# Optimization experiments

Measured on AMD Instinct MI355X. Metric: run time of the kernel, lower is better.

Reference implementation:

```python
import jax, jax.numpy as jnp
import numpy as np

NUM_HEADS = 64  # init kwarg


def _split_heads(x, num_heads):
    # torch: x.view(N, num_heads, head_size).permute(0, 2, 1) -> [N, head_size, num_heads]
    n, hidden = x.shape
    head_size = hidden // num_heads
    return x.reshape(n, num_heads, head_size).transpose(0, 2, 1)


def setup_inputs() -> dict:
    key = jax.random.key(0)
    kq, kk, kv = jax.random.split(key, 3)
    N, H = 4096, 4096
    q = jax.random.normal(kq, (N, H), dtype=jnp.float32)
    k = jax.random.normal(kk, (N, H), dtype=jnp.float32)
    v = jax.random.normal(kv, (N, H), dtype=jnp.float32)
    return {"q": q, "k": k, "v": v}


def reference(q, k, v):
    n, hidden = q.shape
    qh = _split_heads(q, NUM_HEADS)  # [N, d, h] with d=head_size, h=num_heads
    kh = _split_heads(k, NUM_HEADS)
    vh = _split_heads(v, NUM_HEADS)
    # scores: contraction over the num_heads axis (faithful to the original code)
    scores = jnp.einsum('ndh,neh->nde', qh, kh)      # [N, d, d]
    probs = jax.nn.softmax(scores, axis=-1)           # softmax over last dim, no scaling
    out = jnp.einsum('nde,neh->ndh', probs, vh)       # [N, d, h]
    # permute(0,2,1) then flatten -> [N, hidden]
    return out.transpose(0, 2, 1).reshape(n, hidden)
```

## Files before the change

kernel.cpp:

```cpp
#include <hip/hip_runtime.h>
#include <hip/hip_bf16.h>

typedef __bf16 bf16x8 __attribute__((ext_vector_type(8)));
typedef float  f32x4  __attribute__((ext_vector_type(4)));
typedef short  s16x8  __attribute__((ext_vector_type(8)));
typedef unsigned short u16;

static __device__ __forceinline__ u16 f2bf_rne(float f) {
  union { float f; unsigned u; } x; x.f = f;
  unsigned r = x.u + 0x7fffu + ((x.u >> 16) & 1u);
  return (u16)(r >> 16);
}

static __device__ __forceinline__ void splitbf(float f, short& hi, short& lo) {
  union { float f; unsigned u; } x; x.f = f;
  hi = (short)(x.u >> 16);
  union { unsigned u; float f; } h; h.u = x.u & 0xffff0000u;
  union { float f; unsigned u; } y; y.f = f - h.f;
  lo = (short)(y.u >> 16);
}

__global__ __launch_bounds__(256, 2)
void attn64_kernel(const float* __restrict__ q, const float* __restrict__ k,
                   const float* __restrict__ v, float* __restrict__ out)
{
  __shared__ u16 plds[4][4608];
  const int tid  = threadIdx.x;
  const int wid  = tid >> 6;
  const int lane = tid & 63;
  const int quad = lane >> 4;
  const int lo   = lane & 15;
  const int row  = blockIdx.x * 4 + wid;

  u16* P = plds[wid];
  const float* qrow = q + (size_t)row * 4096;
  const float* krow = k + (size_t)row * 4096;
  const float* vrow = v + (size_t)row * 4096;
  float*       orow = out + (size_t)row * 4096;

  const int hq = quad * 8;

  float xk[8][8];
#pragma unroll
  for (int ks = 0; ks < 2; ++ks)
#pragma unroll
    for (int et = 0; et < 4; ++et)
#pragma unroll
      for (int j = 0; j < 8; ++j)
        xk[ks * 4 + et][j] = krow[(ks * 32 + hq + j) * 64 + lo + 16 * et];

  s16x8 kh[8], kl[8];
#pragma unroll
  for (int i = 0; i < 8; ++i)
#pragma unroll
    for (int j = 0; j < 8; ++j) {
      short h0, l0; splitbf(xk[i][j], h0, l0);
      kh[i][j] = h0; kl[i][j] = l0;
    }

  float xq[8][8];
#pragma unroll
  for (int ks = 0; ks < 2; ++ks)
#pragma unroll
    for (int dt = 0; dt < 4; ++dt)
#pragma unroll
      for (int j = 0; j < 8; ++j)
        xq[ks * 4 + dt][j] = qrow[(ks * 32 + hq + j) * 64 + lo + 16 * dt];

  s16x8 qh[8], ql[8];
#pragma unroll
  for (int i = 0; i < 8; ++i)
#pragma unroll
    for (int j = 0; j < 8; ++j) {
      short h0, l0; splitbf(xq[i][j], h0, l0);
      qh[i][j] = h0; ql[i][j] = l0;
    }

  f32x4 xv[8][2];
#pragma unroll
  for (int ks = 0; ks < 2; ++ks)
#pragma unroll
    for (int mt = 0; mt < 4; ++mt) {
      const float* p = vrow + (lo + 16 * mt) * 64 + quad * 8 + ks * 32;
      xv[ks * 4 + mt][0] = *(const f32x4*)p;
      xv[ks * 4 + mt][1] = *(const f32x4*)(p + 4);
    }

  f32x4 acc[4][4];
#pragma unroll
  for (int i = 0; i < 4; ++i)
#pragma unroll
    for (int j = 0; j < 4; ++j) acc[i][j] = (f32x4){0.f, 0.f, 0.f, 0.f};

#pragma unroll
  for (int ks = 0; ks < 2; ++ks)
#pragma unroll
    for (int dt = 0; dt < 4; ++dt) {
      bf16x8 ah = __builtin_bit_cast(bf16x8, qh[ks * 4 + dt]);
      bf16x8 al = __builtin_bit_cast(bf16x8, ql[ks * 4 + dt]);
#pragma unroll
      for (int et = 0; et < 4; ++et) {
        bf16x8 bh = __builtin_bit_cast(bf16x8, kh[ks * 4 + et]);
        bf16x8 bl = __builtin_bit_cast(bf16x8, kl[ks * 4 + et]);
        acc[dt][et] = __builtin_amdgcn_mfma_f32_16x16x32_bf16(ah, bh, acc[dt][et], 0, 0, 0);
        acc[dt][et] = __builtin_amdgcn_mfma_f32_16x16x32_bf16(ah, bl, acc[dt][et], 0, 0, 0);
        acc[dt][et] = __builtin_amdgcn_mfma_f32_16x16x32_bf16(al, bh, acc[dt][et], 0, 0, 0);
      }
    }

#pragma unroll
  for (int dt = 0; dt < 4; ++dt)
#pragma unroll
    for (int r = 0; r < 4; ++r) {
      float m = fmaxf(fmaxf(acc[dt][0][r], acc[dt][1][r]),
                      fmaxf(acc[dt][2][r], acc[dt][3][r]));
#pragma unroll
      for (int off = 1; off < 16; off <<= 1) m = fmaxf(m, __shfl_xor(m, off));
      float s = 0.f;
#pragma unroll
      for (int et = 0; et < 4; ++et) {
        float e0 = __expf(acc[dt][et][r] - m);
        acc[dt][et][r] = e0;
        s += e0;
      }
#pragma unroll
      for (int off = 1; off < 16; off <<= 1) s += __shfl_xor(s, off);
      float rs = 1.0f / s;
#pragma unroll
      for (int et = 0; et < 4; ++et) acc[dt][et][r] *= rs;
    }

  bf16x8 av[8];
#pragma unroll
  for (int i = 0; i < 8; ++i) {
    s16x8 t;
#pragma unroll
    for (int j = 0; j < 4; ++j) {
      t[j]     = (short)f2bf_rne(xv[i][0][j]);
      t[4 + j] = (short)f2bf_rne(xv[i][1][j]);
    }
    av[i] = __builtin_bit_cast(bf16x8, t);
  }

#pragma unroll
  for (int dt = 0; dt < 4; ++dt)
#pragma unroll
    for (int r = 0; r < 4; ++r) {
      const int d = quad * 4 + r + 16 * dt;
#pragma unroll
      for (int et = 0; et < 4; ++et)
        P[d * 72 + lo + 16 * et] = f2bf_rne(acc[dt][et][r]);
    }

  f32x4 acc2[4][4];
#pragma unroll
  for (int i = 0; i < 4; ++i)
#pragma unroll
    for (int j = 0; j < 4; ++j) acc2[i][j] = (f32x4){0.f, 0.f, 0.f, 0.f};

#pragma unroll
  for (int ks = 0; ks < 2; ++ks) {
    bf16x8 bp[4];
#pragma unroll
    for (int nt = 0; nt < 4; ++nt)
      bp[nt] = *(const bf16x8*)&P[(lo + 16 * nt) * 72 + quad * 8 + ks * 32];
#pragma unroll
    for (int mt = 0; mt < 4; ++mt)
#pragma unroll
      for (int nt = 0; nt < 4; ++nt)
        acc2[mt][nt] = __builtin_amdgcn_mfma_f32_16x16x32_bf16(av[ks * 4 + mt], bp[nt], acc2[mt][nt], 0, 0, 0);
  }

#pragma unroll
  for (int mt = 0; mt < 4; ++mt)
#pragma unroll
    for (int r = 0; r < 4; ++r) {
      const int h = quad * 4 + r + 16 * mt;
#pragma unroll
      for (int nt = 0; nt < 4; ++nt)
        orow[h * 64 + lo + 16 * nt] = acc2[mt][nt][r];
    }
}

extern "C" void kernel_launch(void* const* d_in, const int* in_sizes, int n_in,
                              void* d_out, int out_size, void* d_ws, size_t ws_size,
                              hipStream_t stream) {
  const float* q = (const float*)d_in[0];
  const float* k = (const float*)d_in[1];
  const float* v = (const float*)d_in[2];
  float* o = (float*)d_out;
  hipLaunchKernelGGL(attn64_kernel, dim3(1024), dim3(256), 0, stream, q, k, v, o);
}
```

Baseline: 223.8 us.

## Stage Q/K/V rows in LDS via direct global-to-LDS loads, one row per block

Each block now handles a single row with its four waves splitting the 64 d-columns, instead of one row per wave. Q, K and V are copied straight into swizzled LDS with global_load_lds 16-byte transfers, replacing the strided per-lane global gathers. Probabilities are kept as fp32 in LDS, reusing the K buffer, and converted to bf16 on read. The aim is coalesced loads, lower register pressure and higher occupancy (launch bounds raised to 3, grid of 4096 blocks). In exchange it adds two block-wide barriers and uses 48KB of LDS per block, which may cap how many blocks fit per CU.

New measurement: 213.4 us. -4.6%, faster.

```diff
diff --git a/kernel.cpp b/kernel.cpp
--- a/kernel.cpp
+++ b/kernel.cpp
@@ -20,165 +20,160 @@
   lo = (short)(y.u >> 16);
 }
 
-__global__ __launch_bounds__(256, 2)
+#define GLD_LDS16(g, l)                                                        \
+  __builtin_amdgcn_global_load_lds(                                            \
+      (const __attribute__((address_space(1))) void*)(g),                      \
+      (__attribute__((address_space(3))) void*)(l), 16, 0, 0)
+
+__global__ __launch_bounds__(256, 3)
 void attn64_kernel(const float* __restrict__ q, const float* __restrict__ k,
                    const float* __restrict__ v, float* __restrict__ out)
 {
-  __shared__ u16 plds[4][4608];
+  __shared__ float ldsQ[4096];
+  __shared__ float ldsK[4096];
+  __shared__ float ldsV[4096];
+
   const int tid  = threadIdx.x;
   const int wid  = tid >> 6;
   const int lane = tid & 63;
   const int quad = lane >> 4;
   const int lo   = lane & 15;
-  const int row  = blockIdx.x * 4 + wid;
+  const int row  = blockIdx.x;
 
-  u16* P = plds[wid];
   const float* qrow = q + (size_t)row * 4096;
   const float* krow = k + (size_t)row * 4096;
   const float* vrow = v + (size_t)row * 4096;
   float*       orow = out + (size_t)row * 4096;
 
-  const int hq = quad * 8;
+  {
+    const int hl = lane >> 4;
+    const int e4 = (lane & 15) << 2;
+#pragma unroll
+    for (int i = 0; i < 4; ++i) {
+      const int c = wid * 4 + i;
+      const int h = c * 4 + hl;
+      const int seQK = e4 ^ (((h >> 3) & 1) << 4);
+      const int seV  = e4 ^ ((h & 15) << 2);
+      GLD_LDS16(qrow + h * 64 + seQK, &ldsQ[c * 256]);
+      GLD_LDS16(krow + h * 64 + seQK, &ldsK[c * 256]);
+      GLD_LDS16(vrow + h * 64 + seV,  &ldsV[c * 256]);
+    }
+  }
+  __syncthreads();
 
-  float xk[8][8];
+  s16x8 qh[2], ql[2];
+  {
+    const int dcol = wid * 16 + lo;
 #pragma unroll
-  for (int ks = 0; ks < 2; ++ks)
+    for (int ks = 0; ks < 2; ++ks)
 #pragma unroll
-    for (int et = 0; et < 4; ++et)
+      for (int j = 0; j < 8; ++j) {
+        const int h = ks * 32 + quad * 8 + j;
+        float x = ldsQ[h * 64 + (dcol ^ ((quad & 1) << 4))];
+        short hh, ll; splitbf(x, hh, ll);
+        qh[ks][j] = hh; ql[ks][j] = ll;
+      }
+  }
+
+  f32x4 acc[4];
 #pragma unroll
-      for (int j = 0; j < 8; ++j)
-        xk[ks * 4 + et][j] = krow[(ks * 32 + hq + j) * 64 + lo + 16 * et];
-
-  s16x8 kh[8], kl[8];
-#pragma unroll
-  for (int i = 0; i < 8; ++i)
-#pragma unroll
-    for (int j = 0; j < 8; ++j) {
-      short h0, l0; splitbf(xk[i][j], h0, l0);
-      kh[i][j] = h0; kl[i][j] = l0;
-    }
-
-  float xq[8][8];
-#pragma unroll
-  for (int ks = 0; ks < 2; ++ks)
-#pragma unroll
-    for (int dt = 0; dt < 4; ++dt)
-#pragma unroll
-      for (int j = 0; j < 8; ++j)
-        xq[ks * 4 + dt][j] = qrow[(ks * 32 + hq + j) * 64 + lo + 16 * dt];
-
-  s16x8 qh[8], ql[8];
-#pragma unroll
-  for (int i = 0; i < 8; ++i)
-#pragma unroll
-    for (int j = 0; j < 8; ++j) {
-      short h0, l0; splitbf(xq[i][j], h0, l0);
-      qh[i][j] = h0; ql[i][j] = l0;
-    }
-
-  f32x4 xv[8][2];
-#pragma unroll
-  for (int ks = 0; ks < 2; ++ks)
-#pragma unroll
-    for (int mt = 0; mt < 4; ++mt) {
-      const float* p = vrow + (lo + 16 * mt) * 64 + quad * 8 + ks * 32;
-      xv[ks * 4 + mt][0] = *(const f32x4*)p;
-      xv[ks * 4 + mt][1] = *(const f32x4*)(p + 4);
-    }
-
-  f32x4 acc[4][4];
-#pragma unroll
-  for (int i = 0; i < 4; ++i)
-#pragma unroll
-    for (int j = 0; j < 4; ++j) acc[i][j] = (f32x4){0.f, 0.f, 0.f, 0.f};
+  for (int et = 0; et < 4; ++et) acc[et] = (f32x4){0.f, 0.f, 0.f, 0.f};
 
 #pragma unroll
-  for (int ks = 0; ks < 2; ++ks)
+  for (int et = 0; et < 4; ++et)
 #pragma unroll
-    for (int dt = 0; dt < 4; ++dt) {
-      bf16x8 ah = __builtin_bit_cast(bf16x8, qh[ks * 4 + dt]);
-      bf16x8 al = __builtin_bit_cast(bf16x8, ql[ks * 4 + dt]);
+    for (int ks = 0; ks < 2; ++ks) {
+      s16x8 kh, kl;
 #pragma unroll
-      for (int et = 0; et < 4; ++et) {
-        bf16x8 bh = __builtin_bit_cast(bf16x8, kh[ks * 4 + et]);
-        bf16x8 bl = __builtin_bit_cast(bf16x8, kl[ks * 4 + et]);
-        acc[dt][et] = __builtin_amdgcn_mfma_f32_16x16x32_bf16(ah, bh, acc[dt][et], 0, 0, 0);
-        acc[dt][et] = __builtin_amdgcn_mfma_f32_16x16x32_bf16(ah, bl, acc[dt][et], 0, 0, 0);
-        acc[dt][et] = __builtin_amdgcn_mfma_f32_16x16x32_bf16(al, bh, acc[dt][et], 0, 0, 0);
+      for (int j = 0; j < 8; ++j) {
+        const int h = ks * 32 + quad * 8 + j;
+        float x = ldsK[h * 64 + ((lo + 16 * et) ^ ((quad & 1) << 4))];
+        short hh, ll; splitbf(x, hh, ll);
+        kh[j] = hh; kl[j] = ll;
       }
+      bf16x8 ah = __builtin_bit_cast(bf16x8, qh[ks]);
+      bf16x8 al = __builtin_bit_cast(bf16x8, ql[ks]);
+      bf16x8 bh = __builtin_bit_cast(bf16x8, kh);
+      bf16x8 bl = __builtin_bit_cast(bf16x8, kl);
+      acc[et] = __builtin_amdgcn_mfma_f32_16x16x32_bf16(ah, bh, acc[et], 0, 0, 0);
+      acc[et] = __builtin_amdgcn_mfma_f32_16x16x32_bf16(ah, bl, acc[et], 0, 0, 0);
+      acc[et] = __builtin_amdgcn_mfma_f32_16x16x32_bf16(al, bh, acc[et], 0, 0, 0);
     }
 
 #pragma unroll
-  for (int dt = 0; dt < 4; ++dt)
+  for (int r = 0; r < 4; ++r) {
+    float m = fmaxf(fmaxf(acc[0][r], acc[1][r]), fmaxf(acc[2][r], acc[3][r]));
 #pragma unroll
-    for (int r = 0; r < 4; ++r) {
-      float m = fmaxf(fmaxf(acc[dt][0][r], acc[dt][1][r]),
-                      fmaxf(acc[dt][2][r], acc[dt][3][r]));
+    for (int off = 1; off < 16; off <<= 1) m = fmaxf(m, __shfl_xor(m, off));
+    float s = 0.f;
 #pragma unroll
-      for (int off = 1; off < 16; off <<= 1) m = fmaxf(m, __shfl_xor(m, off));
-      float s = 0.f;
+    for (int et = 0; et < 4; ++et) {
+      float e0 = __expf(acc[et][r] - m);
+      acc[et][r] = e0;
+      s += e0;
+    }
 #pragma unroll
-      for (int et = 0; et < 4; ++et) {
-        float e0 = __expf(acc[dt][et][r] - m);
-        acc[dt][et][r] = e0;
-        s += e0;
-      }
+    for (int off = 1; off < 16; off <<= 1) s += __shfl_xor(s, off);
+    float rs = 1.0f / s;
 #pragma unroll
-      for (int off = 1; off < 16; off <<= 1) s += __shfl_xor(s, off);
-      float rs = 1.0f / s;
-#pragma unroll
-      for (int et = 0; et < 4; ++et) acc[dt][et][r] *= rs;
-    }
-
-  bf16x8 av[8];
-#pragma unroll
-  for (int i = 0; i < 8; ++i) {
-    s16x8 t;
-#pragma unroll
-    for (int j = 0; j < 4; ++j) {
-      t[j]     = (short)f2bf_rne(xv[i][0][j]);
-      t[4 + j] = (short)f2bf_rne(xv[i][1][j]);
-    }
-    av[i] = __builtin_bit_cast(bf16x8, t);
+    for (int et = 0; et < 4; ++et) acc[et][r] *= rs;
   }
 
+  __syncthreads();
+
+  float* P = ldsK;
 #pragma unroll
-  for (int dt = 0; dt < 4; ++dt)
+  for (int r = 0; r < 4; ++r) {
+    const int d   = wid * 16 + quad * 4 + r;
+    const int swz = (d & 15) << 2;
 #pragma unroll
-    for (int r = 0; r < 4; ++r) {
-      const int d = quad * 4 + r + 16 * dt;
+    for (int et = 0; et < 4; ++et)
+      P[d * 64 + ((lo + 16 * et) ^ swz)] = acc[et][r];
+  }
+
+  f32x4 acc2[4];
 #pragma unroll
-      for (int et = 0; et < 4; ++et)
-        P[d * 72 + lo + 16 * et] = f2bf_rne(acc[dt][et][r]);
-    }
-
-  f32x4 acc2[4][4];
-#pragma unroll
-  for (int i = 0; i < 4; ++i)
-#pragma unroll
-    for (int j = 0; j < 4; ++j) acc2[i][j] = (f32x4){0.f, 0.f, 0.f, 0.f};
+  for (int mt = 0; mt < 4; ++mt) acc2[mt] = (f32x4){0.f, 0.f, 0.f, 0.f};
 
 #pragma unroll
   for (int ks = 0; ks < 2; ++ks) {
-    bf16x8 bp[4];
+    const int eb = quad * 8 + ks * 32;
+
+    const int dmine = wid * 16 + lo;
+    const int pswz  = lo << 2;
+    f32x4 p0 = *(const f32x4*)&P[dmine * 64 + (eb ^ pswz)];
+    f32x4 p1 = *(const f32x4*)&P[dmine * 64 + ((eb + 4) ^ pswz)];
+    s16x8 tp;
 #pragma unroll
-    for (int nt = 0; nt < 4; ++nt)
-      bp[nt] = *(const bf16x8*)&P[(lo + 16 * nt) * 72 + quad * 8 + ks * 32];
+    for (int j = 0; j < 4; ++j) {
+      tp[j]     = (short)f2bf_rne(p0[j]);
+      tp[4 + j] = (short)f2bf_rne(p1[j]);
+    }
+    bf16x8 bp = __builtin_bit_cast(bf16x8, tp);
+
 #pragma unroll
-    for (int mt = 0; mt < 4; ++mt)
+    for (int mt = 0; mt < 4; ++mt) {
+      const int h    = lo + 16 * mt;
+      const int vswz = lo << 2;
+      f32x4 v0 = *(const f32x4*)&ldsV[h * 64 + (eb ^ vswz)];
+      f32x4 v1 = *(const f32x4*)&ldsV[h * 64 + ((eb + 4) ^ vswz)];
+      s16x8 tv;
 #pragma unroll
-      for (int nt = 0; nt < 4; ++nt)
-        acc2[mt][nt] = __builtin_amdgcn_mfma_f32_16x16x32_bf16(av[ks * 4 + mt], bp[nt], acc2[mt][nt], 0, 0, 0);
+      for (int j = 0; j < 4; ++j) {
+        tv[j]     = (short)f2bf_rne(v0[j]);
+        tv[4 + j] = (short)f2bf_rne(v1[j]);
+      }
+      bf16x8 av = __builtin_bit_cast(bf16x8, tv);
+      acc2[mt] = __builtin_amdgcn_mfma_f32_16x16x32_bf16(av, bp, acc2[mt], 0, 0, 0);
+    }
   }
 
 #pragma unroll
   for (int mt = 0; mt < 4; ++mt)
 #pragma unroll
     for (int r = 0; r < 4; ++r) {
-      const int h = quad * 4 + r + 16 * mt;
-#pragma unroll
-      for (int nt = 0; nt < 4; ++nt)
-        orow[h * 64 + lo + 16 * nt] = acc2[mt][nt][r];
+      const int h = 16 * mt + quad * 4 + r;
+      orow[h * 64 + wid * 16 + lo] = acc2[mt][r];
     }
 }
 
@@ -189,5 +184,5 @@
   const float* k = (const float*)d_in[1];
   const float* v = (const float*)d_in[2];
   float* o = (float*)d_out;
-  hipLaunchKernelGGL(attn64_kernel, dim3(1024), dim3(256), 0, stream, q, k, v, o);
+  hipLaunchKernelGGL(attn64_kernel, dim3(4096), dim3(256), 0, stream, q, k, v, o);
 }
```
